# Performance work log

Hardware: AMD Instinct MI355X
Metric: run time of the kernel (lower is better)

The kernel has to match this reference:

```python
import jax, jax.numpy as jnp
import numpy as np


def setup_inputs() -> dict:
    key = jax.random.key(0)
    k_x, k_W, k_b, k_ids, k_w = jax.random.split(key, 5)
    N_ADAPTERS, D_OUT, D_IN = 32, 1024, 1024
    B, S = 2, 2048
    K = 8  # number of active adapters
    x = jax.random.normal(k_x, (B, S, D_IN), dtype=jnp.float32)
    W = jax.random.normal(k_W, (N_ADAPTERS, D_OUT, D_IN), dtype=jnp.float32)
    b = jax.random.normal(k_b, (N_ADAPTERS, D_OUT), dtype=jnp.float32)
    ids = jax.random.randint(k_ids, (K,), 0, N_ADAPTERS, dtype=jnp.int64)
    weights = jax.random.uniform(k_w, (K,), dtype=jnp.float32)
    return {"x": x, "W": W, "b": b, "ids": ids, "weights": weights}


def reference(x, W, b, ids, weights):
    # Original: out_i = Linear_{ids[i]}(x); output = sum_i weights[i] * out_i
    Wsel = W[ids]  # [k, o, d]  gather of selected adapter weights
    bsel = b[ids]  # [k, o]
    # Fused weighted mixture of k small GEMMs (same math as loop + weighted sum)
    out = jnp.einsum("k,kod,bsd->bso", weights, Wsel, x)
    out = out + jnp.einsum("k,ko->o", weights, bsel)
    return out
```

## Files before the change

### kernel.cpp

```cpp
#include <hip/hip_runtime.h>
#include <hip/hip_bf16.h>
#include <stdint.h>


typedef __attribute__((ext_vector_type(8))) short short8;
typedef __attribute__((ext_vector_type(4))) float float4v;

#define DIMK 1024
#define DIMN 1024
#define DIMM 4096

__device__ __forceinline__ unsigned short f2bf_rtn(float f) {
  union { float f; unsigned u; } v; v.f = f;
  unsigned u = v.u;
  return (unsigned short)((u + 0x7fffu + ((u >> 16) & 1u)) >> 16);
}

__global__ __launch_bounds__(256) void prep_kernel(
    const float* __restrict__ x, const float* __restrict__ W,
    const float* __restrict__ bia, const int* __restrict__ ids,
    const float* __restrict__ wts,
    unsigned short* __restrict__ xb, unsigned short* __restrict__ Wc,
    float* __restrict__ bc, int K)
{
  const int bid = blockIdx.x;
  if (bid < 1024) {
    const int t  = bid * 256 + threadIdx.x;
    const int o  = t >> 8;
    const int d4 = (t & 255) << 2;
    float ax = 0.f, ay = 0.f, az = 0.f, aw = 0.f;
    for (int k = 0; k < K; ++k) {
      const float wk = wts[k];
      const float4 w4 = *reinterpret_cast<const float4*>(
          &W[((size_t)ids[k] << 20) + ((size_t)o << 10) + d4]);
      ax += wk * w4.x; ay += wk * w4.y; az += wk * w4.z; aw += wk * w4.w;
    }
    ushort4 r;
    r.x = f2bf_rtn(ax); r.y = f2bf_rtn(ay); r.z = f2bf_rtn(az); r.w = f2bf_rtn(aw);
    *reinterpret_cast<ushort4*>(&Wc[(size_t)t << 2]) = r;
    if (t < DIMN) {
      float s = 0.f;
      for (int k = 0; k < K; ++k) s += wts[k] * bia[ids[k] * DIMN + t];
      bc[t] = s;
    }
  } else {
    const size_t t = (size_t)(bid - 1024) * 256 + threadIdx.x;
    const float4 v0 = *reinterpret_cast<const float4*>(&x[t << 3]);
    const float4 v1 = *reinterpret_cast<const float4*>(&x[(t << 3) + 4]);
    ushort4 r0, r1;
    r0.x = f2bf_rtn(v0.x); r0.y = f2bf_rtn(v0.y); r0.z = f2bf_rtn(v0.z); r0.w = f2bf_rtn(v0.w);
    r1.x = f2bf_rtn(v1.x); r1.y = f2bf_rtn(v1.y); r1.z = f2bf_rtn(v1.z); r1.w = f2bf_rtn(v1.w);
    *reinterpret_cast<ushort4*>(&xb[t << 3]) = r0;
    *reinterpret_cast<ushort4*>(&xb[(t << 3) + 4]) = r1;
  }
}

__device__ __forceinline__ void load_lds16(const void* g, void* l) {
  __builtin_amdgcn_global_load_lds(
      (const __attribute__((address_space(1))) void*)g,
      (__attribute__((address_space(3))) void*)l, 16, 0, 0);
}

__global__ __launch_bounds__(256) void gemm_kernel(
    const unsigned short* __restrict__ xb,
    const unsigned short* __restrict__ Wc,
    const float* __restrict__ bc,
    float* __restrict__ out)
{
  constexpr int BK = 64;
  constexpr int BM = 128;
  constexpr int BN = 128;
  __shared__ __align__(16) unsigned short As[2][BM * BK];
  __shared__ __align__(16) unsigned short Bs[2][BN * BK];

  const int tid  = threadIdx.x;
  const int wave = tid >> 6;
  const int lane = tid & 63;
  const int m0 = blockIdx.y * BM;
  const int n0 = blockIdx.x * BN;

  const int srow = lane >> 3;
  const int scol = (((lane & 7) ^ srow) << 3);
  const unsigned short* gA = xb + (size_t)(m0 + wave * 32 + srow) * DIMK + scol;
  const unsigned short* gB = Wc + (size_t)(n0 + wave * 32 + srow) * DIMK + scol;

  const int wm   = (wave >> 1) * 64;
  const int wn   = (wave & 1) * 64;
  const int quad = lane >> 4;
  const int r16  = lane & 15;
  const int rx   = r16 & 7;
  const int po0  = ((quad ^ rx) << 3);
  const int po1  = (((4 + quad) ^ rx) << 3);

  const float4v zero = {0.f, 0.f, 0.f, 0.f};
  float4v acc[4][4];
#pragma unroll
  for (int i = 0; i < 4; ++i)
#pragma unroll
    for (int j = 0; j < 4; ++j) acc[i][j] = zero;

#define STAGE(buf, k0)                                                         \
  do {                                                                         \
    _Pragma("unroll")                                                          \
    for (int c = 0; c < 4; ++c) {                                              \
      load_lds16(gA + (size_t)(k0) + (size_t)c * 8 * DIMK,                     \
                 &As[buf][(wave * 32 + c * 8) * BK]);                          \
      load_lds16(gB + (size_t)(k0) + (size_t)c * 8 * DIMK,                     \
                 &Bs[buf][(wave * 32 + c * 8) * BK]);                          \
    }                                                                          \
  } while (0)

#define COMPUTE(buf)                                                           \
  do {                                                                         \
    _Pragma("unroll")                                                          \
    for (int s = 0; s < 2; ++s) {                                              \
      const int po = s ? po1 : po0;                                            \
      short8 af[4], bf[4];                                                     \
      _Pragma("unroll")                                                        \
      for (int mt = 0; mt < 4; ++mt)                                           \
        af[mt] = *reinterpret_cast<const short8*>(                             \
            &As[buf][(wm + mt * 16 + r16) * BK + po]);                         \
      _Pragma("unroll")                                                        \
      for (int nt = 0; nt < 4; ++nt)                                           \
        bf[nt] = *reinterpret_cast<const short8*>(                             \
            &Bs[buf][(wn + nt * 16 + r16) * BK + po]);                         \
      _Pragma("unroll")                                                        \
      for (int mt = 0; mt < 4; ++mt)                                           \
        _Pragma("unroll")                                                      \
        for (int nt = 0; nt < 4; ++nt)                                         \
          acc[mt][nt] = __builtin_amdgcn_mfma_f32_16x16x32_bf16(               \
              af[mt], bf[nt], acc[mt][nt], 0, 0, 0);                           \
    }                                                                          \
  } while (0)

  STAGE(0, 0);
  __syncthreads();

  for (int t = 0; t < DIMK / BK; t += 2) {
    STAGE(1, (t + 1) * BK);
    COMPUTE(0);
    __syncthreads();
    if (t + 2 < DIMK / BK) STAGE(0, (t + 2) * BK);
    COMPUTE(1);
    __syncthreads();
  }

#undef STAGE
#undef COMPUTE

#pragma unroll
  for (int nt = 0; nt < 4; ++nt) {
    const int col = n0 + wn + nt * 16 + r16;
    const float bias = bc[col];
#pragma unroll
    for (int mt = 0; mt < 4; ++mt) {
      const int rbase = m0 + wm + mt * 16 + quad * 4;
#pragma unroll
      for (int r = 0; r < 4; ++r)
        out[(size_t)(rbase + r) * DIMN + col] = acc[mt][nt][r] + bias;
    }
  }
}

extern "C" void kernel_launch(void* const* d_in, const int* in_sizes, int n_in,
                              void* d_out, int out_size, void* d_ws, size_t ws_size,
                              hipStream_t stream) {
  const float* x   = (const float*)d_in[0];
  const float* W   = (const float*)d_in[1];
  const float* b   = (const float*)d_in[2];
  const int*   ids = (const int*)d_in[3];
  const float* wts = (const float*)d_in[4];
  float* out = (float*)d_out;
  const int K = in_sizes[3];

  unsigned short* xb = (unsigned short*)d_ws;
  unsigned short* Wc = (unsigned short*)((char*)d_ws + (8u << 20));
  float*          bc = (float*)((char*)d_ws + (10u << 20));

  prep_kernel<<<3072, 256, 0, stream>>>(x, W, b, ids, wts, xb, Wc, bc, K);
  dim3 grid(DIMN / 128, DIMM / 128);
  gemm_kernel<<<grid, 256, 0, stream>>>(xb, Wc, bc, out);
}
```

Before: 209.7 us.

## Fuse x fp32-to-bf16 conversion into GEMM A-tile loading, shrink M tile

The separate conversion pass over x into a bf16 workspace is removed. The GEMM now loads fp32 x rows into registers, converts them to bf16 and writes them into swizzled LDS, overlapped with the MFMA compute of the other buffer. This avoids one full write and read of the 8 MB bf16 copy of x. The M tile shrinks to 64, doubling the grid, and launch bounds ask for 2 blocks per CU. The cost is that fp32 A reads are twice as large per tile, conversion ALU work now sits inside the GEMM, and more blocks re-read the same Wc data.

New measurement: 212.3 us. No clear change (+1.2%).

```diff
diff --git a/kernel.cpp b/kernel.cpp
--- a/kernel.cpp
+++ b/kernel.cpp
@@ -4,6 +4,7 @@
 
 
 typedef __attribute__((ext_vector_type(8))) short short8;
+typedef __attribute__((ext_vector_type(8))) unsigned short ushort8;
 typedef __attribute__((ext_vector_type(4))) float float4v;
 
 #define DIMK 1024
@@ -17,41 +18,27 @@
 }
 
 __global__ __launch_bounds__(256) void prep_kernel(
-    const float* __restrict__ x, const float* __restrict__ W,
-    const float* __restrict__ bia, const int* __restrict__ ids,
-    const float* __restrict__ wts,
-    unsigned short* __restrict__ xb, unsigned short* __restrict__ Wc,
-    float* __restrict__ bc, int K)
+    const float* __restrict__ W, const float* __restrict__ bia,
+    const int* __restrict__ ids, const float* __restrict__ wts,
+    unsigned short* __restrict__ Wc, float* __restrict__ bc, int K)
 {
-  const int bid = blockIdx.x;
-  if (bid < 1024) {
-    const int t  = bid * 256 + threadIdx.x;
-    const int o  = t >> 8;
-    const int d4 = (t & 255) << 2;
-    float ax = 0.f, ay = 0.f, az = 0.f, aw = 0.f;
-    for (int k = 0; k < K; ++k) {
-      const float wk = wts[k];
-      const float4 w4 = *reinterpret_cast<const float4*>(
-          &W[((size_t)ids[k] << 20) + ((size_t)o << 10) + d4]);
-      ax += wk * w4.x; ay += wk * w4.y; az += wk * w4.z; aw += wk * w4.w;
-    }
-    ushort4 r;
-    r.x = f2bf_rtn(ax); r.y = f2bf_rtn(ay); r.z = f2bf_rtn(az); r.w = f2bf_rtn(aw);
-    *reinterpret_cast<ushort4*>(&Wc[(size_t)t << 2]) = r;
-    if (t < DIMN) {
-      float s = 0.f;
-      for (int k = 0; k < K; ++k) s += wts[k] * bia[ids[k] * DIMN + t];
-      bc[t] = s;
-    }
-  } else {
-    const size_t t = (size_t)(bid - 1024) * 256 + threadIdx.x;
-    const float4 v0 = *reinterpret_cast<const float4*>(&x[t << 3]);
-    const float4 v1 = *reinterpret_cast<const float4*>(&x[(t << 3) + 4]);
-    ushort4 r0, r1;
-    r0.x = f2bf_rtn(v0.x); r0.y = f2bf_rtn(v0.y); r0.z = f2bf_rtn(v0.z); r0.w = f2bf_rtn(v0.w);
-    r1.x = f2bf_rtn(v1.x); r1.y = f2bf_rtn(v1.y); r1.z = f2bf_rtn(v1.z); r1.w = f2bf_rtn(v1.w);
-    *reinterpret_cast<ushort4*>(&xb[t << 3]) = r0;
-    *reinterpret_cast<ushort4*>(&xb[(t << 3) + 4]) = r1;
+  const int t  = blockIdx.x * 256 + threadIdx.x;
+  const int o  = t >> 8;
+  const int d4 = (t & 255) << 2;
+  float ax = 0.f, ay = 0.f, az = 0.f, aw = 0.f;
+  for (int k = 0; k < K; ++k) {
+    const float wk = wts[k];
+    const float4 w4 = *reinterpret_cast<const float4*>(
+        &W[((size_t)ids[k] << 20) + ((size_t)o << 10) + d4]);
+    ax += wk * w4.x; ay += wk * w4.y; az += wk * w4.z; aw += wk * w4.w;
+  }
+  ushort4 r;
+  r.x = f2bf_rtn(ax); r.y = f2bf_rtn(ay); r.z = f2bf_rtn(az); r.w = f2bf_rtn(aw);
+  *reinterpret_cast<ushort4*>(&Wc[(size_t)t << 2]) = r;
+  if (t < DIMN) {
+    float s = 0.f;
+    for (int k = 0; k < K; ++k) s += wts[k] * bia[ids[k] * DIMN + t];
+    bc[t] = s;
   }
 }
 
@@ -61,30 +48,33 @@
       (__attribute__((address_space(3))) void*)l, 16, 0, 0);
 }
 
-__global__ __launch_bounds__(256) void gemm_kernel(
-    const unsigned short* __restrict__ xb,
+__global__ __launch_bounds__(256, 2) void gemm_kernel(
+    const float* __restrict__ x,
     const unsigned short* __restrict__ Wc,
     const float* __restrict__ bc,
     float* __restrict__ out)
 {
   constexpr int BK = 64;
-  constexpr int BM = 128;
-  constexpr int BN = 128;
-  __shared__ __align__(16) unsigned short As[2][BM * BK];
-  __shared__ __align__(16) unsigned short Bs[2][BN * BK];
+  __shared__ __align__(16) unsigned short As[2][64 * BK];
+  __shared__ __align__(16) unsigned short Bs[2][128 * BK];
 
   const int tid  = threadIdx.x;
   const int wave = tid >> 6;
   const int lane = tid & 63;
-  const int m0 = blockIdx.y * BM;
-  const int n0 = blockIdx.x * BN;
+  const int m0 = blockIdx.y * 64;
+  const int n0 = blockIdx.x * 128;
 
   const int srow = lane >> 3;
   const int scol = (((lane & 7) ^ srow) << 3);
-  const unsigned short* gA = xb + (size_t)(m0 + wave * 32 + srow) * DIMK + scol;
   const unsigned short* gB = Wc + (size_t)(n0 + wave * 32 + srow) * DIMK + scol;
 
-  const int wm   = (wave >> 1) * 64;
+  const int arow = tid >> 3;
+  const int ag   = tid & 7;
+  const int asw  = ((ag ^ (arow & 7)) << 3);
+  const float* gxa = x + (size_t)(m0 + arow) * DIMK + (ag << 3);
+  float4 aR[4];
+
+  const int wm   = (wave >> 1) * 32;
   const int wn   = (wave & 1) * 64;
   const int quad = lane >> 4;
   const int r16  = lane & 15;
@@ -93,21 +83,42 @@
   const int po1  = (((4 + quad) ^ rx) << 3);
 
   const float4v zero = {0.f, 0.f, 0.f, 0.f};
-  float4v acc[4][4];
-#pragma unroll
-  for (int i = 0; i < 4; ++i)
+  float4v acc[2][4];
+#pragma unroll
+  for (int i = 0; i < 2; ++i)
 #pragma unroll
     for (int j = 0; j < 4; ++j) acc[i][j] = zero;
 
-#define STAGE(buf, k0)                                                         \
+#define LOADA(kk)                                                              \
+  do {                                                                         \
+    const float* p = gxa + (size_t)(kk) * BK;                                  \
+    aR[0] = *reinterpret_cast<const float4*>(p);                               \
+    aR[1] = *reinterpret_cast<const float4*>(p + 4);                           \
+    aR[2] = *reinterpret_cast<const float4*>(p + 32 * DIMK);                   \
+    aR[3] = *reinterpret_cast<const float4*>(p + 32 * DIMK + 4);               \
+  } while (0)
+
+#define CVTWRITE(buf)                                                          \
+  do {                                                                         \
+    ushort8 w0, w1;                                                            \
+    w0[0] = f2bf_rtn(aR[0].x); w0[1] = f2bf_rtn(aR[0].y);                      \
+    w0[2] = f2bf_rtn(aR[0].z); w0[3] = f2bf_rtn(aR[0].w);                      \
+    w0[4] = f2bf_rtn(aR[1].x); w0[5] = f2bf_rtn(aR[1].y);                      \
+    w0[6] = f2bf_rtn(aR[1].z); w0[7] = f2bf_rtn(aR[1].w);                      \
+    w1[0] = f2bf_rtn(aR[2].x); w1[1] = f2bf_rtn(aR[2].y);                      \
+    w1[2] = f2bf_rtn(aR[2].z); w1[3] = f2bf_rtn(aR[2].w);                      \
+    w1[4] = f2bf_rtn(aR[3].x); w1[5] = f2bf_rtn(aR[3].y);                      \
+    w1[6] = f2bf_rtn(aR[3].z); w1[7] = f2bf_rtn(aR[3].w);                      \
+    *reinterpret_cast<ushort8*>(&As[buf][arow * BK + asw]) = w0;               \
+    *reinterpret_cast<ushort8*>(&As[buf][(arow + 32) * BK + asw]) = w1;        \
+  } while (0)
+
+#define STAGEB(buf, kstep)                                                     \
   do {                                                                         \
     _Pragma("unroll")                                                          \
-    for (int c = 0; c < 4; ++c) {                                              \
-      load_lds16(gA + (size_t)(k0) + (size_t)c * 8 * DIMK,                     \
-                 &As[buf][(wave * 32 + c * 8) * BK]);                          \
-      load_lds16(gB + (size_t)(k0) + (size_t)c * 8 * DIMK,                     \
+    for (int c = 0; c < 4; ++c)                                                \
+      load_lds16(gB + (size_t)(kstep) * BK + (size_t)c * 8 * DIMK,             \
                  &Bs[buf][(wave * 32 + c * 8) * BK]);                          \
-    }                                                                          \
   } while (0)
 
 #define COMPUTE(buf)                                                           \
@@ -115,9 +126,9 @@
     _Pragma("unroll")                                                          \
     for (int s = 0; s < 2; ++s) {                                              \
       const int po = s ? po1 : po0;                                            \
-      short8 af[4], bf[4];                                                     \
+      short8 af[2], bf[4];                                                     \
       _Pragma("unroll")                                                        \
-      for (int mt = 0; mt < 4; ++mt)                                           \
+      for (int mt = 0; mt < 2; ++mt)                                           \
         af[mt] = *reinterpret_cast<const short8*>(                             \
             &As[buf][(wm + mt * 16 + r16) * BK + po]);                         \
       _Pragma("unroll")                                                        \
@@ -125,7 +136,7 @@
         bf[nt] = *reinterpret_cast<const short8*>(                             \
             &Bs[buf][(wn + nt * 16 + r16) * BK + po]);                         \
       _Pragma("unroll")                                                        \
-      for (int mt = 0; mt < 4; ++mt)                                           \
+      for (int mt = 0; mt < 2; ++mt)                                           \
         _Pragma("unroll")                                                      \
         for (int nt = 0; nt < 4; ++nt)                                         \
           acc[mt][nt] = __builtin_amdgcn_mfma_f32_16x16x32_bf16(               \
@@ -133,19 +144,26 @@
     }                                                                          \
   } while (0)
 
-  STAGE(0, 0);
+  LOADA(0);
+  STAGEB(0, 0);
+  CVTWRITE(0);
   __syncthreads();
 
   for (int t = 0; t < DIMK / BK; t += 2) {
-    STAGE(1, (t + 1) * BK);
+    LOADA(t + 1);
+    STAGEB(1, t + 1);
     COMPUTE(0);
+    CVTWRITE(1);
     __syncthreads();
-    if (t + 2 < DIMK / BK) STAGE(0, (t + 2) * BK);
+    if (t + 2 < DIMK / BK) { LOADA(t + 2); STAGEB(0, t + 2); }
     COMPUTE(1);
+    if (t + 2 < DIMK / BK) CVTWRITE(0);
     __syncthreads();
   }
 
-#undef STAGE
+#undef LOADA
+#undef CVTWRITE
+#undef STAGEB
 #undef COMPUTE
 
 #pragma unroll
@@ -153,7 +171,7 @@
     const int col = n0 + wn + nt * 16 + r16;
     const float bias = bc[col];
 #pragma unroll
-    for (int mt = 0; mt < 4; ++mt) {
+    for (int mt = 0; mt < 2; ++mt) {
       const int rbase = m0 + wm + mt * 16 + quad * 4;
 #pragma unroll
       for (int r = 0; r < 4; ++r)
@@ -173,11 +191,10 @@
   float* out = (float*)d_out;
   const int K = in_sizes[3];
 
-  unsigned short* xb = (unsigned short*)d_ws;
-  unsigned short* Wc = (unsigned short*)((char*)d_ws + (8u << 20));
-  float*          bc = (float*)((char*)d_ws + (10u << 20));
-
-  prep_kernel<<<3072, 256, 0, stream>>>(x, W, b, ids, wts, xb, Wc, bc, K);
-  dim3 grid(DIMN / 128, DIMM / 128);
-  gemm_kernel<<<grid, 256, 0, stream>>>(xb, Wc, bc, out);
-}
+  unsigned short* Wc = (unsigned short*)d_ws;
+  float*          bc = (float*)((char*)d_ws + (2u << 20));
+
+  prep_kernel<<<1024, 256, 0, stream>>>(W, b, ids, wts, Wc, bc, K);
+  dim3 grid(DIMN / 128, DIMM / 64);
+  gemm_kernel<<<grid, 256, 0, stream>>>(x, Wc, bc, out);
+}
```
